# Performance work log

Measured on AMD Instinct MI355X. Metric: run time of the kernel, lower is better.

The kernel has to match this reference:

```python
import jax, jax.numpy as jnp
import numpy as np


def setup_inputs() -> dict:
    key = jax.random.key(0)
    k1, k2, k3, k4, k5 = jax.random.split(key, 5)
    B, S, I, O, R = 4, 2048, 4096, 4096, 16
    s = 1.0 / np.sqrt(I)
    return {
        "x": jax.random.normal(k1, (B, S, I), dtype=jnp.float32),
        "W": jax.random.normal(k2, (O, I), dtype=jnp.float32) * s,
        "b": jax.random.normal(k3, (O,), dtype=jnp.float32) * 0.02,
        "lora_A": jax.random.normal(k4, (I, R), dtype=jnp.float32) * s,
        "lora_B": jax.random.normal(k5, (R, O), dtype=jnp.float32) * 0.02,
    }


def reference(x, W, b, lora_A, lora_B):
    # Base linear: F.linear(x, W, b) = x @ W.T + b   -> [B, S, O]
    base_out = jnp.einsum("bsi,oi->bso", x, W) + b
    # LoRA low-rank delta: (x @ A) @ B  -> [B, S, O]
    lora_out = jnp.einsum("bsr,ro->bso", jnp.einsum("bsi,ir->bsr", x, lora_A), lora_B)
    return base_out + lora_out
```

## Files before the change

kernel.cpp:

```cpp
#include <hip/hip_runtime.h>

typedef float f32x4 __attribute__((ext_vector_type(4)));
typedef __bf16 bf16x8 __attribute__((ext_vector_type(8)));
typedef __bf16 bf16x4 __attribute__((ext_vector_type(4)));

#define GLOBAL_AS __attribute__((address_space(1)))
#define LDS_AS    __attribute__((address_space(3)))

static __device__ __forceinline__ void gload16(const void* g, void* l) {
  __builtin_amdgcn_global_load_lds((const GLOBAL_AS void*)g, (LDS_AS void*)l, 16, 0, 0);
}

#define BAR() __builtin_amdgcn_s_barrier()
#define WAITL0() do { asm volatile("s_waitcnt lgkmcnt(0)" ::: "memory"); __builtin_amdgcn_sched_barrier(0); } while (0)

__global__ __launch_bounds__(256)
void xa_cvt(const float* __restrict__ X, const float* __restrict__ A,
            __bf16* __restrict__ Xb, __bf16* __restrict__ XAb) {
  constexpr int K = 4096, TM = 16, KC = 64;
  __shared__ float Xs[TM][68];
  __shared__ float At[16][68];
  const int t = threadIdx.x;
  const int m0 = blockIdx.x * TM;
  const int lrow = t >> 4, c4 = (t & 15) * 4;
  const int orow = t >> 4, oc = t & 15;
  const int akk = t >> 2, ar4 = (t & 3) * 4;
  f32x4 av = (f32x4)0.f;
  for (int k0 = 0; k0 < K; k0 += KC) {
    const float* gx = X + (size_t)(m0 + lrow) * K + k0 + c4;
    f32x4 u = *reinterpret_cast<const f32x4*>(gx);
    *reinterpret_cast<f32x4*>(&Xs[lrow][c4]) = u;
    bf16x4 p;
#pragma unroll
    for (int e = 0; e < 4; ++e) p[e] = (__bf16)u[e];
    *reinterpret_cast<bf16x4*>(Xb + (size_t)(m0 + lrow) * K + k0 + c4) = p;
    f32x4 a = *reinterpret_cast<const f32x4*>(A + (size_t)(k0 + akk) * 16 + ar4);
    At[ar4 + 0][akk] = a[0]; At[ar4 + 1][akk] = a[1];
    At[ar4 + 2][akk] = a[2]; At[ar4 + 3][akk] = a[3];
    __syncthreads();
#pragma unroll
    for (int q = 0; q < 16; ++q) {
      f32x4 xv = *reinterpret_cast<const f32x4*>(&Xs[orow][q * 4]);
      av += xv * *reinterpret_cast<const f32x4*>(&At[oc][q * 4]);
    }
    __syncthreads();
  }
  const float acc = av[0] + av[1] + av[2] + av[3];
  const size_t base = (size_t)(m0 + orow) * 64;
  XAb[base + oc] = (__bf16)acc;
#pragma unroll
  for (int z = 0; z < 3; ++z) XAb[base + 16 + z * 16 + oc] = (__bf16)0.f;
}

__global__ __launch_bounds__(256)
void cvt_f32_bf16(const float* __restrict__ in, __bf16* __restrict__ out, long n8) {
  long i = (long)blockIdx.x * blockDim.x + threadIdx.x;
  long stride = (long)gridDim.x * blockDim.x;
  for (; i < n8; i += stride) {
    f32x4 u = reinterpret_cast<const f32x4*>(in)[2 * i];
    f32x4 v = reinterpret_cast<const f32x4*>(in)[2 * i + 1];
    bf16x8 p;
#pragma unroll
    for (int e = 0; e < 4; ++e) { p[e] = (__bf16)u[e]; p[4 + e] = (__bf16)v[e]; }
    reinterpret_cast<bf16x8*>(out)[i] = p;
  }
}

__global__ __launch_bounds__(256)
void blt64(const float* __restrict__ Bl, __bf16* __restrict__ BlT) {
  int idx = blockIdx.x * 256 + threadIdx.x;
  int col = idx >> 6, k = idx & 63;
  float v = (k < 16) ? Bl[(size_t)k * 4096 + col] : 0.f;
  BlT[idx] = (__bf16)v;
}

__global__ __launch_bounds__(512, 2)
void gemm8(const __bf16* __restrict__ Xb, const __bf16* __restrict__ Wb,
           const __bf16* __restrict__ XAb, const __bf16* __restrict__ BlT,
           const float* __restrict__ bias, float* __restrict__ out) {
  constexpr int N = 4096, K = 4096;
  __shared__ __align__(16) char sm[131072];
  char* Asm_ = sm;
  char* Bsm_ = sm + 65536;

  const int t = threadIdx.x;
  const int lane = t & 63, w = t >> 6;
  const int wr = w >> 2, wc = w & 3;
  const int fr = lane & 15, fg = lane >> 4;

  const int bid = blockIdx.x;
  const int xcd = bid & 7, l = bid >> 3;
  const int mt = (xcd << 2) | ((l >> 4) & 2) | (l & 1);
  const int nt = (l >> 1) & 15;
  const int m0 = mt * 256, n0 = nt * 256;

  const int sRow = w * 16 + (lane >> 2);
  const int sColB = (((lane & 3) ^ ((lane >> 3) & 3)) << 4);
  const int rdOff = fr * 64 + ((fg ^ ((fr >> 1) & 3)) << 4);
  const int rdOffA = wr * 16384 + rdOff;
  const int rdOffB = (wc >> 1) * 16384 + (wc & 1) * 8192 + rdOff;

  auto stageA = [&](int h, int tt) {
    char* dst = Asm_ + (tt & 1) * 32768 + h * 16384 + w * 2048;
    const char* g;
    if (tt < 64) g = (const char*)(Xb + (size_t)(m0 + h * 128 + sRow) * K + (size_t)tt * 64) + sColB;
    else         g = (const char*)(XAb + (size_t)(m0 + h * 128 + sRow) * 64) + sColB;
    gload16(g, dst);
    gload16(g + 64, dst + 1024);
  };
  auto stageB = [&](int h, int tt) {
    char* dst = Bsm_ + (tt & 1) * 32768 + h * 16384 + w * 2048;
    const char* g;
    if (tt < 64) g = (const char*)(Wb + (size_t)(n0 + h * 128 + sRow) * K + (size_t)tt * 64) + sColB;
    else         g = (const char*)(BlT + (size_t)(n0 + h * 128 + sRow) * 64) + sColB;
    gload16(g, dst);
    gload16(g + 64, dst + 1024);
  };

  auto rdA = [&](int b, int mf, int kk) -> bf16x8 {
    return *reinterpret_cast<const bf16x8*>(Asm_ + b * 32768 + (mf * 2 + kk) * 1024 + rdOffA);
  };
  auto rdB = [&](int b, int nf, int kk) -> bf16x8 {
    return *reinterpret_cast<const bf16x8*>(Bsm_ + b * 32768 + (nf * 2 + kk) * 1024 + rdOffB);
  };

  f32x4 acc[8][4];
#pragma unroll
  for (int i = 0; i < 8; ++i)
#pragma unroll
    for (int j = 0; j < 4; ++j) acc[i][j] = (f32x4)0.f;

  bf16x8 aF[4][2], bL[2][2], bH[2][2];

  auto MF = [&](bf16x8 (&af)[4][2], bf16x8 (&bf_)[2][2], int mi, int ni) {
#pragma unroll
    for (int i = 0; i < 4; ++i)
#pragma unroll
      for (int j = 0; j < 2; ++j)
#pragma unroll
        for (int kk = 0; kk < 2; ++kk)
          acc[mi * 4 + i][ni * 2 + j] = __builtin_amdgcn_mfma_f32_16x16x32_bf16(
              af[i][kk], bf_[j][kk], acc[mi * 4 + i][ni * 2 + j], 0, 0, 0);
  };

  auto tile_step = [&](int tv) {
    const int b = tv & 1;
#pragma unroll
    for (int i = 0; i < 4; ++i)
#pragma unroll
      for (int kk = 0; kk < 2; ++kk) aF[i][kk] = rdA(b, i, kk);
#pragma unroll
    for (int j = 0; j < 2; ++j)
#pragma unroll
      for (int kk = 0; kk < 2; ++kk) bL[j][kk] = rdB(b, j, kk);
    BAR(); WAITL0();
    __builtin_amdgcn_s_setprio(1); MF(aF, bL, 0, 0); __builtin_amdgcn_s_setprio(0);
    BAR();
#pragma unroll
    for (int j = 0; j < 2; ++j)
#pragma unroll
      for (int kk = 0; kk < 2; ++kk) bH[j][kk] = rdB(b, 2 + j, kk);
    BAR(); WAITL0();
    __builtin_amdgcn_s_setprio(1); MF(aF, bH, 0, 1); __builtin_amdgcn_s_setprio(0);
    BAR();
#pragma unroll
    for (int i = 0; i < 4; ++i)
#pragma unroll
      for (int kk = 0; kk < 2; ++kk) aF[i][kk] = rdA(b, 4 + i, kk);
    stageB(0, tv + 2);
    stageB(1, tv + 2);
    BAR(); WAITL0();
    __builtin_amdgcn_s_setprio(1); MF(aF, bH, 1, 1); __builtin_amdgcn_s_setprio(0);
    BAR();
    stageA(0, tv + 2);
    stageA(1, tv + 2);
    BAR(); WAITL0();
    __builtin_amdgcn_s_setprio(1); MF(aF, bL, 1, 0); __builtin_amdgcn_s_setprio(0);
    asm volatile("s_waitcnt vmcnt(8)" ::: "memory");
    BAR();
  };

  stageB(0, 0); stageB(1, 0); stageA(0, 0); stageA(1, 0);
  stageB(0, 1); stageB(1, 1); stageA(0, 1); stageA(1, 1);
  asm volatile("s_waitcnt vmcnt(8)" ::: "memory");
  BAR();

  for (int tv = 0; tv < 63; ++tv) tile_step(tv);

  {
    const int b = 1;
#pragma unroll
    for (int i = 0; i < 4; ++i)
#pragma unroll
      for (int kk = 0; kk < 2; ++kk) aF[i][kk] = rdA(b, i, kk);
#pragma unroll
    for (int j = 0; j < 2; ++j)
#pragma unroll
      for (int kk = 0; kk < 2; ++kk) bL[j][kk] = rdB(b, j, kk);
    BAR(); WAITL0();
    __builtin_amdgcn_s_setprio(1); MF(aF, bL, 0, 0); __builtin_amdgcn_s_setprio(0);
    BAR();
#pragma unroll
    for (int j = 0; j < 2; ++j)
#pragma unroll
      for (int kk = 0; kk < 2; ++kk) bH[j][kk] = rdB(b, 2 + j, kk);
    BAR(); WAITL0();
    __builtin_amdgcn_s_setprio(1); MF(aF, bH, 0, 1); __builtin_amdgcn_s_setprio(0);
    BAR();
#pragma unroll
    for (int i = 0; i < 4; ++i)
#pragma unroll
      for (int kk = 0; kk < 2; ++kk) aF[i][kk] = rdA(b, 4 + i, kk);
    BAR(); WAITL0();
    __builtin_amdgcn_s_setprio(1); MF(aF, bH, 1, 1); __builtin_amdgcn_s_setprio(0);
    BAR();
    __builtin_amdgcn_s_setprio(1); MF(aF, bL, 1, 0); __builtin_amdgcn_s_setprio(0);
    asm volatile("s_waitcnt vmcnt(0)" ::: "memory");
    BAR();
  }

  {
#pragma unroll
    for (int i = 0; i < 4; ++i)
#pragma unroll
      for (int kk = 0; kk < 2; ++kk) aF[i][kk] = rdA(0, i, kk);
#pragma unroll
    for (int j = 0; j < 2; ++j)
#pragma unroll
      for (int kk = 0; kk < 2; ++kk) { bL[j][kk] = rdB(0, j, kk); bH[j][kk] = rdB(0, 2 + j, kk); }
    MF(aF, bL, 0, 0); MF(aF, bH, 0, 1);
#pragma unroll
    for (int i = 0; i < 4; ++i)
#pragma unroll
      for (int kk = 0; kk < 2; ++kk) aF[i][kk] = rdA(0, 4 + i, kk);
    MF(aF, bH, 1, 1); MF(aF, bL, 1, 0);
  }

  float bb[4];
#pragma unroll
  for (int j = 0; j < 4; ++j) bb[j] = bias[n0 + wc * 64 + j * 16 + fr];
#pragma unroll
  for (int i = 0; i < 8; ++i) {
    const int row0 = m0 + wr * 128 + i * 16 + fg * 4;
#pragma unroll
    for (int j = 0; j < 4; ++j) {
      const int col = n0 + wc * 64 + j * 16 + fr;
#pragma unroll
      for (int q = 0; q < 4; ++q)
        out[(size_t)(row0 + q) * N + col] = acc[i][j][q] + bb[j];
    }
  }
}

extern "C" void kernel_launch(void* const* d_in, const int* in_sizes, int n_in,
                              void* d_out, int out_size, void* d_ws, size_t ws_size,
                              hipStream_t stream) {
  const float* x  = (const float*)d_in[0];
  const float* W  = (const float*)d_in[1];
  const float* b  = (const float*)d_in[2];
  const float* lA = (const float*)d_in[3];
  const float* lB = (const float*)d_in[4];
  float* out = (float*)d_out;

  char* ws = (char*)d_ws;
  __bf16* Xb  = (__bf16*)ws;
  __bf16* Wb  = (__bf16*)(ws + 67108864);
  __bf16* XAb = (__bf16*)(ws + 100663296);
  __bf16* BlT = (__bf16*)(ws + 101711872);

  xa_cvt<<<8192 / 16, 256, 0, stream>>>(x, lA, Xb, XAb);
  cvt_f32_bf16<<<1024, 256, 0, stream>>>(W, Wb, (long)4096 * 4096 / 8);
  blt64<<<4096 * 64 / 256, 256, 0, stream>>>(lB, BlT);

  gemm8<<<dim3(512), dim3(512), 0, stream>>>(Xb, Wb, XAb, BlT, b, out);
}
```

Measured before the change: 338.1 us.

## Merge prep kernels into one launch and restage GEMM pipeline with precomputed pointers

Combines the X/XA conversion, W conversion and LoRA-B transpose into a single launch with block-range dispatch, which removes two kernel launches and the gaps between them. In the GEMM, the per-stage global pointers are precomputed and advanced incrementally, so the branchy stage lambdas go away. Loads are spread across all four MFMA phases, with A and B staged into alternating buffers at different offsets, and the LoRA tiles get peeled epilogue steps. The pipeline wait counts change, so the synchronisation carries more correctness risk.

```diff
diff --git a/kernel.cpp b/kernel.cpp
--- a/kernel.cpp
+++ b/kernel.cpp
@@ -15,63 +15,62 @@
 #define WAITL0() do { asm volatile("s_waitcnt lgkmcnt(0)" ::: "memory"); __builtin_amdgcn_sched_barrier(0); } while (0)
 
 __global__ __launch_bounds__(256)
-void xa_cvt(const float* __restrict__ X, const float* __restrict__ A,
-            __bf16* __restrict__ Xb, __bf16* __restrict__ XAb) {
-  constexpr int K = 4096, TM = 16, KC = 64;
-  __shared__ float Xs[TM][68];
+void prep_all(const float* __restrict__ X, const float* __restrict__ A,
+              const float* __restrict__ W, const float* __restrict__ Bl,
+              __bf16* __restrict__ Xb, __bf16* __restrict__ XAb,
+              __bf16* __restrict__ Wb, __bf16* __restrict__ BlT) {
+  __shared__ float Xs[16][68];
   __shared__ float At[16][68];
+  const int bid = blockIdx.x;
   const int t = threadIdx.x;
-  const int m0 = blockIdx.x * TM;
-  const int lrow = t >> 4, c4 = (t & 15) * 4;
-  const int orow = t >> 4, oc = t & 15;
-  const int akk = t >> 2, ar4 = (t & 3) * 4;
-  f32x4 av = (f32x4)0.f;
-  for (int k0 = 0; k0 < K; k0 += KC) {
-    const float* gx = X + (size_t)(m0 + lrow) * K + k0 + c4;
-    f32x4 u = *reinterpret_cast<const f32x4*>(gx);
-    *reinterpret_cast<f32x4*>(&Xs[lrow][c4]) = u;
-    bf16x4 p;
-#pragma unroll
-    for (int e = 0; e < 4; ++e) p[e] = (__bf16)u[e];
-    *reinterpret_cast<bf16x4*>(Xb + (size_t)(m0 + lrow) * K + k0 + c4) = p;
-    f32x4 a = *reinterpret_cast<const f32x4*>(A + (size_t)(k0 + akk) * 16 + ar4);
-    At[ar4 + 0][akk] = a[0]; At[ar4 + 1][akk] = a[1];
-    At[ar4 + 2][akk] = a[2]; At[ar4 + 3][akk] = a[3];
-    __syncthreads();
-#pragma unroll
-    for (int q = 0; q < 16; ++q) {
-      f32x4 xv = *reinterpret_cast<const f32x4*>(&Xs[orow][q * 4]);
-      av += xv * *reinterpret_cast<const f32x4*>(&At[oc][q * 4]);
+  if (bid < 512) {
+    constexpr int K = 4096, KC = 64;
+    const int m0 = bid * 16;
+    const int lrow = t >> 4, c4 = (t & 15) * 4;
+    const int orow = t >> 4, oc = t & 15;
+    const int akk = t >> 2, ar4 = (t & 3) * 4;
+    f32x4 av = (f32x4)0.f;
+    for (int k0 = 0; k0 < K; k0 += KC) {
+      f32x4 u = *reinterpret_cast<const f32x4*>(X + (size_t)(m0 + lrow) * K + k0 + c4);
+      *reinterpret_cast<f32x4*>(&Xs[lrow][c4]) = u;
+      bf16x4 p;
+#pragma unroll
+      for (int e = 0; e < 4; ++e) p[e] = (__bf16)u[e];
+      *reinterpret_cast<bf16x4*>(Xb + (size_t)(m0 + lrow) * K + k0 + c4) = p;
+      f32x4 a = *reinterpret_cast<const f32x4*>(A + (size_t)(k0 + akk) * 16 + ar4);
+      At[ar4 + 0][akk] = a[0]; At[ar4 + 1][akk] = a[1];
+      At[ar4 + 2][akk] = a[2]; At[ar4 + 3][akk] = a[3];
+      __syncthreads();
+#pragma unroll
+      for (int q = 0; q < 16; ++q) {
+        f32x4 xv = *reinterpret_cast<const f32x4*>(&Xs[orow][q * 4]);
+        av += xv * *reinterpret_cast<const f32x4*>(&At[oc][q * 4]);
+      }
+      __syncthreads();
     }
-    __syncthreads();
-  }
-  const float acc = av[0] + av[1] + av[2] + av[3];
-  const size_t base = (size_t)(m0 + orow) * 64;
-  XAb[base + oc] = (__bf16)acc;
-#pragma unroll
-  for (int z = 0; z < 3; ++z) XAb[base + 16 + z * 16 + oc] = (__bf16)0.f;
-}
-
-__global__ __launch_bounds__(256)
-void cvt_f32_bf16(const float* __restrict__ in, __bf16* __restrict__ out, long n8) {
-  long i = (long)blockIdx.x * blockDim.x + threadIdx.x;
-  long stride = (long)gridDim.x * blockDim.x;
-  for (; i < n8; i += stride) {
-    f32x4 u = reinterpret_cast<const f32x4*>(in)[2 * i];
-    f32x4 v = reinterpret_cast<const f32x4*>(in)[2 * i + 1];
-    bf16x8 p;
-#pragma unroll
-    for (int e = 0; e < 4; ++e) { p[e] = (__bf16)u[e]; p[4 + e] = (__bf16)v[e]; }
-    reinterpret_cast<bf16x8*>(out)[i] = p;
-  }
-}
-
-__global__ __launch_bounds__(256)
-void blt64(const float* __restrict__ Bl, __bf16* __restrict__ BlT) {
-  int idx = blockIdx.x * 256 + threadIdx.x;
-  int col = idx >> 6, k = idx & 63;
-  float v = (k < 16) ? Bl[(size_t)k * 4096 + col] : 0.f;
-  BlT[idx] = (__bf16)v;
+    const float acc = av[0] + av[1] + av[2] + av[3];
+    const size_t base = (size_t)(m0 + orow) * 64;
+    XAb[base + oc] = (__bf16)acc;
+#pragma unroll
+    for (int z = 0; z < 3; ++z) XAb[base + 16 + z * 16 + oc] = (__bf16)0.f;
+  } else if (bid < 1536) {
+    long base = (long)(bid - 512) * 256 + t;
+#pragma unroll
+    for (int r = 0; r < 8; ++r) {
+      long i = base + (long)r * 262144;
+      f32x4 u = reinterpret_cast<const f32x4*>(W)[2 * i];
+      f32x4 v = reinterpret_cast<const f32x4*>(W)[2 * i + 1];
+      bf16x8 p;
+#pragma unroll
+      for (int e = 0; e < 4; ++e) { p[e] = (__bf16)u[e]; p[4 + e] = (__bf16)v[e]; }
+      reinterpret_cast<bf16x8*>(Wb)[i] = p;
+    }
+  } else {
+    int idx = (bid - 1536) * 256 + t;
+    int col = idx >> 6, k = idx & 63;
+    float v = (k < 16) ? Bl[(size_t)k * 4096 + col] : 0.f;
+    BlT[idx] = (__bf16)v;
+  }
 }
 
 __global__ __launch_bounds__(512, 2)
@@ -100,22 +99,12 @@
   const int rdOffA = wr * 16384 + rdOff;
   const int rdOffB = (wc >> 1) * 16384 + (wc & 1) * 8192 + rdOff;
 
-  auto stageA = [&](int h, int tt) {
-    char* dst = Asm_ + (tt & 1) * 32768 + h * 16384 + w * 2048;
-    const char* g;
-    if (tt < 64) g = (const char*)(Xb + (size_t)(m0 + h * 128 + sRow) * K + (size_t)tt * 64) + sColB;
-    else         g = (const char*)(XAb + (size_t)(m0 + h * 128 + sRow) * 64) + sColB;
-    gload16(g, dst);
-    gload16(g + 64, dst + 1024);
-  };
-  auto stageB = [&](int h, int tt) {
-    char* dst = Bsm_ + (tt & 1) * 32768 + h * 16384 + w * 2048;
-    const char* g;
-    if (tt < 64) g = (const char*)(Wb + (size_t)(n0 + h * 128 + sRow) * K + (size_t)tt * 64) + sColB;
-    else         g = (const char*)(BlT + (size_t)(n0 + h * 128 + sRow) * 64) + sColB;
-    gload16(g, dst);
-    gload16(g + 64, dst + 1024);
-  };
+  const char* gA0 = (const char*)Xb + (size_t)(m0 + sRow) * 8192 + sColB;
+  const char* gA1 = (const char*)Xb + (size_t)(m0 + 128 + sRow) * 8192 + sColB;
+  const char* gB0 = (const char*)Wb + (size_t)(n0 + sRow) * 8192 + sColB;
+  const char* gB1 = (const char*)Wb + (size_t)(n0 + 128 + sRow) * 8192 + sColB;
+
+  auto stage2 = [&](const char* g, char* dst) { gload16(g, dst); gload16(g + 64, dst + 1024); };
 
   auto rdA = [&](int b, int mf, int kk) -> bf16x8 {
     return *reinterpret_cast<const bf16x8*>(Asm_ + b * 32768 + (mf * 2 + kk) * 1024 + rdOffA);
@@ -143,8 +132,27 @@
               af[i][kk], bf_[j][kk], acc[mi * 4 + i][ni * 2 + j], 0, 0, 0);
   };
 
-  auto tile_step = [&](int tv) {
-    const int b = tv & 1;
+  float bb[4];
+#pragma unroll
+  for (int j = 0; j < 4; ++j) bb[j] = bias[n0 + wc * 64 + j * 16 + fr];
+
+  stage2(gA0, Asm_ + w * 2048);
+  stage2(gA1, Asm_ + 16384 + w * 2048);
+  stage2(gB0, Bsm_ + w * 2048);
+  stage2(gB1, Bsm_ + 16384 + w * 2048);
+  stage2(gB0 + 128, Bsm_ + 32768 + w * 2048);
+  stage2(gB1 + 128, Bsm_ + 32768 + 16384 + w * 2048);
+  asm volatile("s_waitcnt vmcnt(4)" ::: "memory");
+  BAR();
+
+  const char* pA0 = gA0 + 128;
+  const char* pA1 = gA1 + 128;
+  const char* pB0 = gB0 + 256;
+  const char* pB1 = gB1 + 256;
+
+  auto tile_step = [&](int b) {
+    char* dstA = Asm_ + (b ^ 1) * 32768 + w * 2048;
+    char* dstB = Bsm_ + b * 32768 + w * 2048;
 #pragma unroll
     for (int i = 0; i < 4; ++i)
 #pragma unroll
@@ -153,6 +161,8 @@
     for (int j = 0; j < 2; ++j)
 #pragma unroll
       for (int kk = 0; kk < 2; ++kk) bL[j][kk] = rdB(b, j, kk);
+    stage2(pA0, dstA); pA0 += 128;
+    asm volatile("s_waitcnt lgkmcnt(8)" ::: "memory");
     BAR(); WAITL0();
     __builtin_amdgcn_s_setprio(1); MF(aF, bL, 0, 0); __builtin_amdgcn_s_setprio(0);
     BAR();
@@ -160,6 +170,7 @@
     for (int j = 0; j < 2; ++j)
 #pragma unroll
       for (int kk = 0; kk < 2; ++kk) bH[j][kk] = rdB(b, 2 + j, kk);
+    stage2(pA1, dstA + 16384); pA1 += 128;
     BAR(); WAITL0();
     __builtin_amdgcn_s_setprio(1); MF(aF, bH, 0, 1); __builtin_amdgcn_s_setprio(0);
     BAR();
@@ -167,58 +178,98 @@
     for (int i = 0; i < 4; ++i)
 #pragma unroll
       for (int kk = 0; kk < 2; ++kk) aF[i][kk] = rdA(b, 4 + i, kk);
-    stageB(0, tv + 2);
-    stageB(1, tv + 2);
+    stage2(pB0, dstB); pB0 += 128;
     BAR(); WAITL0();
     __builtin_amdgcn_s_setprio(1); MF(aF, bH, 1, 1); __builtin_amdgcn_s_setprio(0);
     BAR();
-    stageA(0, tv + 2);
-    stageA(1, tv + 2);
+    stage2(pB1, dstB + 16384); pB1 += 128;
     BAR(); WAITL0();
     __builtin_amdgcn_s_setprio(1); MF(aF, bL, 1, 0); __builtin_amdgcn_s_setprio(0);
-    asm volatile("s_waitcnt vmcnt(8)" ::: "memory");
+    asm volatile("s_waitcnt vmcnt(4)" ::: "memory");
     BAR();
   };
 
-  stageB(0, 0); stageB(1, 0); stageA(0, 0); stageA(1, 0);
-  stageB(0, 1); stageB(1, 1); stageA(0, 1); stageA(1, 1);
-  asm volatile("s_waitcnt vmcnt(8)" ::: "memory");
+  for (int tp = 0; tp < 31; ++tp) { tile_step(0); tile_step(1); }
+
+  {
+    const char* gBl0 = (const char*)BlT + (size_t)(n0 + sRow) * 128 + sColB;
+    const char* gBl1 = (const char*)BlT + (size_t)(n0 + 128 + sRow) * 128 + sColB;
+    char* dstA = Asm_ + 32768 + w * 2048;
+    char* dstB = Bsm_ + w * 2048;
+#pragma unroll
+    for (int i = 0; i < 4; ++i)
+#pragma unroll
+      for (int kk = 0; kk < 2; ++kk) aF[i][kk] = rdA(0, i, kk);
+#pragma unroll
+    for (int j = 0; j < 2; ++j)
+#pragma unroll
+      for (int kk = 0; kk < 2; ++kk) bL[j][kk] = rdB(0, j, kk);
+    stage2(pA0, dstA);
+    asm volatile("s_waitcnt lgkmcnt(8)" ::: "memory");
+    BAR(); WAITL0();
+    __builtin_amdgcn_s_setprio(1); MF(aF, bL, 0, 0); __builtin_amdgcn_s_setprio(0);
+    BAR();
+#pragma unroll
+    for (int j = 0; j < 2; ++j)
+#pragma unroll
+      for (int kk = 0; kk < 2; ++kk) bH[j][kk] = rdB(0, 2 + j, kk);
+    stage2(pA1, dstA + 16384);
+    BAR(); WAITL0();
+    __builtin_amdgcn_s_setprio(1); MF(aF, bH, 0, 1); __builtin_amdgcn_s_setprio(0);
+    BAR();
+#pragma unroll
+    for (int i = 0; i < 4; ++i)
+#pragma unroll
+      for (int kk = 0; kk < 2; ++kk) aF[i][kk] = rdA(0, 4 + i, kk);
+    stage2(gBl0, dstB);
+    BAR(); WAITL0();
+    __builtin_amdgcn_s_setprio(1); MF(aF, bH, 1, 1); __builtin_amdgcn_s_setprio(0);
+    BAR();
+    stage2(gBl1, dstB + 16384);
+    BAR(); WAITL0();
+    __builtin_amdgcn_s_setprio(1); MF(aF, bL, 1, 0); __builtin_amdgcn_s_setprio(0);
+    asm volatile("s_waitcnt vmcnt(4)" ::: "memory");
+    BAR();
+  }
+
+  {
+    const char* gXA0 = (const char*)XAb + (size_t)(m0 + sRow) * 128 + sColB;
+    const char* gXA1 = (const char*)XAb + (size_t)(m0 + 128 + sRow) * 128 + sColB;
+    char* dstA = Asm_ + w * 2048;
+#pragma unroll
+    for (int i = 0; i < 4; ++i)
+#pragma unroll
+      for (int kk = 0; kk < 2; ++kk) aF[i][kk] = rdA(1, i, kk);
+#pragma unroll
+    for (int j = 0; j < 2; ++j)
+#pragma unroll
+      for (int kk = 0; kk < 2; ++kk) bL[j][kk] = rdB(1, j, kk);
+    stage2(gXA0, dstA);
+    asm volatile("s_waitcnt lgkmcnt(8)" ::: "memory");
+    BAR(); WAITL0();
+    __builtin_amdgcn_s_setprio(1); MF(aF, bL, 0, 0); __builtin_amdgcn_s_setprio(0);
+    BAR();
+#pragma unroll
+    for (int j = 0; j < 2; ++j)
+#pragma unroll
+      for (int kk = 0; kk < 2; ++kk) bH[j][kk] = rdB(1, 2 + j, kk);
+    stage2(gXA1, dstA + 16384);
+    BAR(); WAITL0();
+    __builtin_amdgcn_s_setprio(1); MF(aF, bH, 0, 1); __builtin_amdgcn_s_setprio(0);
+    BAR();
+#pragma unroll
+    for (int i = 0; i < 4; ++i)
+#pragma unroll
+      for (int kk = 0; kk < 2; ++kk) aF[i][kk] = rdA(1, 4 + i, kk);
+    BAR(); WAITL0();
+    __builtin_amdgcn_s_setprio(1); MF(aF, bH, 1, 1); __builtin_amdgcn_s_setprio(0);
+    BAR();
+    __builtin_amdgcn_s_setprio(1); MF(aF, bL, 1, 0); __builtin_amdgcn_s_setprio(0);
+    BAR();
+  }
+
+  asm volatile("s_waitcnt vmcnt(0)" ::: "memory");
   BAR();
-
-  for (int tv = 0; tv < 63; ++tv) tile_step(tv);
-
-  {
-    const int b = 1;
-#pragma unroll
-    for (int i = 0; i < 4; ++i)
-#pragma unroll
-      for (int kk = 0; kk < 2; ++kk) aF[i][kk] = rdA(b, i, kk);
-#pragma unroll
-    for (int j = 0; j < 2; ++j)
-#pragma unroll
-      for (int kk = 0; kk < 2; ++kk) bL[j][kk] = rdB(b, j, kk);
-    BAR(); WAITL0();
-    __builtin_amdgcn_s_setprio(1); MF(aF, bL, 0, 0); __builtin_amdgcn_s_setprio(0);
-    BAR();
-#pragma unroll
-    for (int j = 0; j < 2; ++j)
-#pragma unroll
-      for (int kk = 0; kk < 2; ++kk) bH[j][kk] = rdB(b, 2 + j, kk);
-    BAR(); WAITL0();
-    __builtin_amdgcn_s_setprio(1); MF(aF, bH, 0, 1); __builtin_amdgcn_s_setprio(0);
-    BAR();
-#pragma unroll
-    for (int i = 0; i < 4; ++i)
-#pragma unroll
-      for (int kk = 0; kk < 2; ++kk) aF[i][kk] = rdA(b, 4 + i, kk);
-    BAR(); WAITL0();
-    __builtin_amdgcn_s_setprio(1); MF(aF, bH, 1, 1); __builtin_amdgcn_s_setprio(0);
-    BAR();
-    __builtin_amdgcn_s_setprio(1); MF(aF, bL, 1, 0); __builtin_amdgcn_s_setprio(0);
-    asm volatile("s_waitcnt vmcnt(0)" ::: "memory");
-    BAR();
-  }
-
   {
 #pragma unroll
     for (int i = 0; i < 4; ++i)
@@ -236,9 +287,6 @@
     MF(aF, bH, 1, 1); MF(aF, bL, 1, 0);
   }
 
-  float bb[4];
-#pragma unroll
-  for (int j = 0; j < 4; ++j) bb[j] = bias[n0 + wc * 64 + j * 16 + fr];
 #pragma unroll
   for (int i = 0; i < 8; ++i) {
     const int row0 = m0 + wr * 128 + i * 16 + fg * 4;
@@ -268,9 +316,6 @@
   __bf16* XAb = (__bf16*)(ws + 100663296);
   __bf16* BlT = (__bf16*)(ws + 101711872);
 
-  xa_cvt<<<8192 / 16, 256, 0, stream>>>(x, lA, Xb, XAb);
-  cvt_f32_bf16<<<1024, 256, 0, stream>>>(W, Wb, (long)4096 * 4096 / 8);
-  blt64<<<4096 * 64 / 256, 256, 0, stream>>>(lB, BlT);
-
+  prep_all<<<2560, 256, 0, stream>>>(x, lA, W, lB, Xb, XAb, Wb, BlT);
   gemm8<<<dim3(512), dim3(512), 0, stream>>>(Xb, Wb, XAb, BlT, b, out);
 }
```

Result: faster. 315.8 us (-6.6%).
